# Performance work log

Hardware: AMD Instinct MI355X
Metric: run time of the kernel (lower is better)

The kernel has to match this reference:

```python
import jax, jax.numpy as jnp
import numpy as np

B, H, W, C, NB = 3, 256, 256, 16, 4
EPS = 1e-3  # keras BatchNormalization default epsilon


def _conv(x, w, b):
    y = jax.lax.conv_general_dilated(x, w, (1, 1), 'SAME',
                                     dimension_numbers=('NHWC', 'HWIO', 'NHWC'))
    return y + b


def _bn(x, g, be, mu, v):
    # inference-mode batch norm with moving statistics
    return (x - mu) * jax.lax.rsqrt(v + EPS) * g + be


def _extract_patches(x, p, s):
    # tf.image.extract_patches(..., padding='SAME') -> (b, oh, ow, p, p, c)
    b, h, w, c = x.shape
    oh, ow = -(-h // s), -(-w // s)
    pth = max((oh - 1) * s + p - h, 0)
    ptw = max((ow - 1) * s + p - w, 0)
    xp = jnp.pad(x, ((0, 0), (pth // 2, pth - pth // 2), (ptw // 2, ptw - ptw // 2), (0, 0)))
    ri = np.arange(oh)[:, None] * s + np.arange(p)[None, :]  # (oh, p)
    ci = np.arange(ow)[:, None] * s + np.arange(p)[None, :]  # (ow, p)
    return xp[:, ri[:, None, :, None], ci[None, :, None, :], :]


def setup_inputs() -> dict:
    key = jax.random.key(0)
    ks = jax.random.split(key, 4)
    mr = jax.random.normal(ks[0], (B, H, W, C), jnp.float32)
    pet = jax.random.normal(ks[1], (B, H, W, C), jnp.float32)
    W1 = jax.random.normal(ks[2], (3, 3, C, C * NB), jnp.float32) * 0.05
    W2 = jax.random.normal(ks[3], (3, 3, C * NB, C * NB), jnp.float32) * 0.05
    z = jnp.zeros((C * NB,), jnp.float32)
    o = jnp.ones((C * NB,), jnp.float32)
    return dict(mr_features=mr, pet_features=pet,
                W1=W1, b1=z, g1=o, be1=z, mu1=z, v1=o,
                W2=W2, b2=z, g2=o, be2=z, mu2=z, v2=o,
                patch=8, stride=4)


def reference(mr_features, pet_features, W1, b1, g1, be1, mu1, v1,
              W2, b2, g2, be2, mu2, v2, patch, stride):
    px = py = int(patch)
    sx = sy = int(stride)
    bsz, h, w, c = mr_features.shape

    # ---- B_Kernel_Function_Generator ----
    x = jax.nn.relu(_bn(_conv(mr_features, W1, b1), g1, be1, mu1, v1))
    x = _bn(_conv(x, W2, b2), g2, be2, mu2, v2)  # last conv_block: no activation
    nb = x.shape[-1] // c
    x = x.reshape(bsz, h, w, c, nb)
    x = jax.nn.softmax(x, axis=-1)
    b_features = jnp.where(x > 1e-5, x, 0.0)  # mask * x

    # ---- Sparse_Kernel_Matrix_Multiplication ----
    bc, bf = c, nb
    Nx, Ny = h // px, w // py
    lx, ly = px // sx, py // sy
    SNx, SNy = Nx * lx, Ny * ly

    bflat = b_features.reshape(bsz, h, w, bc * bf)
    bp = _extract_patches(bflat, px, sx).reshape(bsz, SNx, SNy, px, py, bc, bf)
    pp = _extract_patches(pet_features, px, sx).reshape(bsz, SNx, SNy, px, py, bc, 1)

    dn = jnp.sum(bp, axis=(3, 4), keepdims=True)              # diagonal norm
    kp = jnp.sum(pp * bp, axis=(3, 4), keepdims=True)         # kernel-weighted PET
    dn_safe = jnp.where(dn == 0, 1.0, dn)
    kn = jnp.where(dn == 0, 0.0, kp / dn_safe) * bp           # divide_no_nan
    kpet = jnp.sum(kn, axis=-1)                               # (b,SNx,SNy,px,py,bc)

    # deinterleave stride phases: kernel_pet[:, i::lx, j::ly] stack
    kp6 = kpet.reshape(bsz, Nx, lx, Ny, ly, px, py, c)
    st = kp6.transpose(4, 2, 0, 1, 3, 5, 6, 7).reshape(lx * ly, bsz, Nx, Ny, px, py, c)
    t = st.transpose(1, 2, 3, 4, 5, 6, 0).reshape(bsz, Nx, Ny, px, py, c, lx, ly)
    t = t.transpose(0, 1, 3, 2, 4, 5, 6, 7).reshape(bsz, Nx * px, Ny * py, c, lx, ly)
    t = t.transpose(4, 5, 0, 1, 2, 3)  # (lx, ly, b, H, W, c)

    # align_patches: roll each shifted copy back into registration, then mean
    rev = t.transpose(2, 3, 4, 5, 0, 1).reshape(bsz, h, w, c, lx * ly)
    rev = rev.transpose(4, 0, 1, 2, 3)  # (lx*ly, b, H, W, c)
    rollx = np.arange(-px // 2 + sx // 2, px // 2 + sx // 2, sx)
    rolly = np.arange(-py // 2 + sy // 2, py // 2 + sy // 2, sy)
    acc = jnp.zeros((bsz, h, w, c), rev.dtype)
    for m in range(lx * ly):  # small fixed set (lx*ly = 4)
        acc = acc + jnp.roll(rev[m], (int(rollx[m % lx]), int(rolly[m // lx])), axis=(1, 2))
    return acc / (lx * ly)
```

## Files before the change

kernel.cpp:

```cpp
#include <hip/hip_runtime.h>

#define EPSB 1e-3f

typedef _Float16 half8 __attribute__((ext_vector_type(8)));
typedef _Float16 half4 __attribute__((ext_vector_type(4)));
typedef float f32x4 __attribute__((ext_vector_type(4)));

__global__ __launch_bounds__(256, 4)
void k_prep(const float* __restrict__ W1, const float* __restrict__ W2,
            const float* __restrict__ b1, const float* __restrict__ g1,
            const float* __restrict__ be1, const float* __restrict__ mu1,
            const float* __restrict__ v1,
            const float* __restrict__ b2, const float* __restrict__ g2,
            const float* __restrict__ be2, const float* __restrict__ mu2,
            const float* __restrict__ v2,
            _Float16* __restrict__ W1F, _Float16* __restrict__ W2F,
            float* __restrict__ ST)
{
    int t = blockIdx.x * 256 + threadIdx.x;
    if (t < 5 * 4 * 64 * 8) {
        int k = t & 7, lane = (t >> 3) & 63, snt = t >> 9;
        int s = snt >> 2, ct = snt & 3;
        int quad = lane >> 4, n16 = lane & 15;
        int tap = 2 * s + (quad >> 1);
        int ci  = (quad & 1) * 8 + k;
        int co  = ct * 16 + n16;
        float v = (tap < 9) ? W1[(tap * 16 + ci) * 64 + co] : 0.f;
        W1F[t] = (_Float16)v;
        return;
    }
    t -= 5 * 4 * 64 * 8;
    if (t < 18 * 4 * 64 * 8) {
        int k = t & 7, lane = (t >> 3) & 63, snt = t >> 9;
        int s = snt >> 2, ct = snt & 3;
        int quad = lane >> 4, n16 = lane & 15;
        int tap = s >> 1;
        int ci  = (s & 1) * 32 + quad * 8 + k;
        int co  = ct * 16 + n16;
        W2F[t] = (_Float16)W2[(tap * 64 + ci) * 64 + co];
        return;
    }
    t -= 18 * 4 * 64 * 8;
    if (t < 256) {
        int c = t & 63, sel = t >> 6;
        if (sel == 0)      ST[c]       = g1[c] * rsqrtf(v1[c] + EPSB);
        else if (sel == 1) ST[64 + c]  = (b1[c] - mu1[c]) * (g1[c] * rsqrtf(v1[c] + EPSB)) + be1[c];
        else if (sel == 2) ST[128 + c] = g2[c] * rsqrtf(v2[c] + EPSB);
        else               ST[192 + c] = (b2[c] - mu2[c]) * (g2[c] * rsqrtf(v2[c] + EPSB)) + be2[c];
    }
}

#define CIP1 24
__global__ __launch_bounds__(256, 3)
void k_conv1(const float* __restrict__ mr, const _Float16* __restrict__ W1F,
             const float* __restrict__ ST, _Float16* __restrict__ A)
{
    __shared__ __align__(16) _Float16 sIn[6 * 66 * CIP1];
    const int tid = threadIdx.x;
    const int b  = blockIdx.y;
    const int r0 = (blockIdx.x >> 2) * 4;
    const int q0 = (blockIdx.x & 3) * 64;

    for (int idx = tid; idx < 6 * 66 * 2; idx += 256) {
        int c = idx & 1, pp = idx >> 1;
        int p = pp % 66, dy = pp / 66;
        int rr = r0 + dy - 1, qg = q0 + p - 1;
        half8 h = (half8)(_Float16)0.f;
        if ((unsigned)rr < 256u && (unsigned)qg < 256u) {
            const float* src = mr + ((b * 256 + rr) * 256 + qg) * 16 + c * 8;
            float4 v0 = *(const float4*)src;
            float4 v1 = *(const float4*)(src + 4);
            h = (half8){(_Float16)v0.x, (_Float16)v0.y, (_Float16)v0.z, (_Float16)v0.w,
                        (_Float16)v1.x, (_Float16)v1.y, (_Float16)v1.z, (_Float16)v1.w};
        }
        *(half8*)(&sIn[(dy * 66 + p) * CIP1 + c * 8]) = h;
    }
    __syncthreads();

    const int w = tid >> 6, lane = tid & 63;
    const int n16 = lane & 15, quad = lane >> 4;
    const int ci0 = (quad & 1) * 8;

    f32x4 acc[4][4];
    #pragma unroll
    for (int i = 0; i < 4; ++i)
        #pragma unroll
        for (int j = 0; j < 4; ++j) acc[i][j] = (f32x4){0.f, 0.f, 0.f, 0.f};

    #pragma unroll
    for (int s = 0; s < 5; ++s) {
        int tap  = 2 * s + (quad >> 1);
        int tapc = tap > 8 ? 8 : tap;
        int dy = tapc / 3, dx = tapc % 3;
        half8 wfrag[4], pfrag[4];
        #pragma unroll
        for (int ct = 0; ct < 4; ++ct)
            wfrag[ct] = *(const half8*)(W1F + ((s * 4 + ct) * 64 + lane) * 8);
        #pragma unroll
        for (int qt = 0; qt < 4; ++qt)
            pfrag[qt] = *(const half8*)&sIn[((w + dy) * 66 + qt * 16 + n16 + dx) * CIP1 + ci0];
        #pragma unroll
        for (int qt = 0; qt < 4; ++qt)
            #pragma unroll
            for (int ct = 0; ct < 4; ++ct)
                acc[qt][ct] = __builtin_amdgcn_mfma_f32_16x16x32_f16(wfrag[ct], pfrag[qt], acc[qt][ct], 0, 0, 0);
    }

    const int r = r0 + w;
    #pragma unroll
    for (int ct = 0; ct < 4; ++ct) {
        int co0 = ct * 16 + quad * 4;
        f32x4 sc = *(const f32x4*)&ST[co0];
        f32x4 sh = *(const f32x4*)&ST[64 + co0];
        #pragma unroll
        for (int qt = 0; qt < 4; ++qt) {
            int q = q0 + qt * 16 + n16;
            half4 h;
            #pragma unroll
            for (int j = 0; j < 4; ++j)
                h[j] = (_Float16)fmaxf(acc[qt][ct][j] * sc[j] + sh[j], 0.f);
            *(half4*)(A + (((b * 256 + r) * 256 + q) * 64 + co0)) = h;
        }
    }
}

#define CIP2 72
__global__ __launch_bounds__(256, 2)
void k_conv2(const _Float16* __restrict__ A, const _Float16* __restrict__ W2F,
             const float* __restrict__ ST, const float* __restrict__ pet,
             _Float16* __restrict__ BF, float* __restrict__ S2)
{
    __shared__ __align__(16) _Float16 sIn[6 * 66 * CIP2];
    const int tid = threadIdx.x;
    const int b  = blockIdx.y;
    const int r0 = (blockIdx.x >> 2) * 4;
    const int q0 = (blockIdx.x & 3) * 64;

    for (int idx = tid; idx < 6 * 66 * 8; idx += 256) {
        int c = idx & 7, pp = idx >> 3;
        int p = pp % 66, dy = pp / 66;
        int rr = r0 + dy - 1, qg = q0 + p - 1;
        int4 v = {0, 0, 0, 0};
        if ((unsigned)rr < 256u && (unsigned)qg < 256u)
            v = *(const int4*)(A + (((b * 256 + rr) * 256 + qg) * 64 + c * 8));
        *(int4*)(&sIn[(dy * 66 + p) * CIP2 + c * 8]) = v;
    }
    __syncthreads();

    const int w = tid >> 6, lane = tid & 63;
    const int n16 = lane & 15, quad = lane >> 4;

    f32x4 acc[4][4];
    #pragma unroll
    for (int i = 0; i < 4; ++i)
        #pragma unroll
        for (int j = 0; j < 4; ++j) acc[i][j] = (f32x4){0.f, 0.f, 0.f, 0.f};

    #pragma unroll
    for (int s = 0; s < 18; ++s) {
        const int tap = s >> 1;
        const int dy = tap / 3, dx = tap % 3;
        const int ci0 = (s & 1) * 32 + quad * 8;
        half8 wfrag[4], pfrag[4];
        #pragma unroll
        for (int ct = 0; ct < 4; ++ct)
            wfrag[ct] = *(const half8*)(W2F + ((s * 4 + ct) * 64 + lane) * 8);
        #pragma unroll
        for (int qt = 0; qt < 4; ++qt)
            pfrag[qt] = *(const half8*)&sIn[((w + dy) * 66 + qt * 16 + n16 + dx) * CIP2 + ci0];
        #pragma unroll
        for (int qt = 0; qt < 4; ++qt)
            #pragma unroll
            for (int ct = 0; ct < 4; ++ct)
                acc[qt][ct] = __builtin_amdgcn_mfma_f32_16x16x32_f16(wfrag[ct], pfrag[qt], acc[qt][ct], 0, 0, 0);
    }

    const int r = r0 + w;
    half4 hv[4][4];
    #pragma unroll
    for (int ct = 0; ct < 4; ++ct) {
        int co0 = ct * 16 + quad * 4;
        f32x4 sc = *(const f32x4*)&ST[128 + co0];
        f32x4 sh = *(const f32x4*)&ST[192 + co0];
        #pragma unroll
        for (int qt = 0; qt < 4; ++qt) {
            int q = q0 + qt * 16 + n16;
            float z0 = acc[qt][ct][0] * sc[0] + sh[0];
            float z1 = acc[qt][ct][1] * sc[1] + sh[1];
            float z2 = acc[qt][ct][2] * sc[2] + sh[2];
            float z3 = acc[qt][ct][3] * sc[3] + sh[3];
            float mx = fmaxf(fmaxf(z0, z1), fmaxf(z2, z3));
            float e0 = __expf(z0 - mx), e1 = __expf(z1 - mx);
            float e2 = __expf(z2 - mx), e3 = __expf(z3 - mx);
            float inv = __builtin_amdgcn_rcpf((e0 + e1) + (e2 + e3));
            float p0 = e0 * inv, p1 = e1 * inv, p2 = e2 * inv, p3 = e3 * inv;
            half4 h;
            h[0] = (_Float16)(p0 > 1e-5f ? p0 : 0.f);
            h[1] = (_Float16)(p1 > 1e-5f ? p1 : 0.f);
            h[2] = (_Float16)(p2 > 1e-5f ? p2 : 0.f);
            h[3] = (_Float16)(p3 > 1e-5f ? p3 : 0.f);
            hv[ct][qt] = h;
            *(half4*)(BF + (((b * 256 + r) * 256 + q) * 64 + co0)) = h;
        }
    }

    __syncthreads();
    #pragma unroll
    for (int ct = 0; ct < 4; ++ct) {
        int co0 = ct * 16 + quad * 4;
        #pragma unroll
        for (int qt = 0; qt < 4; ++qt) {
            int ql = qt * 16 + n16;
            *(half4*)(&sIn[(w * 64 + ql) * CIP2 + co0]) = hv[ct][qt];
        }
    }
    __syncthreads();

    const int k4 = tid & 3;
    const int cell = tid >> 2;
    const int rp = cell >> 5, qp = cell & 31;
    float dn[16], kp[16];
    #pragma unroll
    for (int j = 0; j < 16; ++j) { dn[j] = 0.f; kp[j] = 0.f; }
    #pragma unroll
    for (int u = 0; u < 2; ++u)
        #pragma unroll
        for (int v = 0; v < 2; ++v) {
            int rl = 2 * rp + u, ql = 2 * qp + v;
            half8 b0 = *(const half8*)(&sIn[(rl * 64 + ql) * CIP2 + k4 * 16]);
            half8 b1 = *(const half8*)(&sIn[(rl * 64 + ql) * CIP2 + k4 * 16 + 8]);
            float4 p4 = *(const float4*)(pet + ((b * 256 + r0 + rl) * 256 + q0 + ql) * 16 + 4 * k4);
            #pragma unroll
            for (int j = 0; j < 8; ++j) {
                float bv = (float)b0[j];
                dn[j] += bv;
                kp[j] = fmaf((j < 4) ? p4.x : p4.y, bv, kp[j]);
            }
            #pragma unroll
            for (int j = 0; j < 8; ++j) {
                float bv = (float)b1[j];
                dn[8 + j] += bv;
                kp[8 + j] = fmaf((j < 4) ? p4.z : p4.w, bv, kp[8 + j]);
            }
        }
    float* o = S2 + 2 * ((size_t)(((b * 128 + (r0 >> 1) + rp) * 128 + (q0 >> 1) + qp) * 64) + 16 * k4);
    #pragma unroll
    for (int m = 0; m < 8; ++m)
        *(float4*)(o + 4 * m) = make_float4(dn[2*m], kp[2*m], dn[2*m+1], kp[2*m+1]);
}

__global__ __launch_bounds__(256, 4)
void k_ratio(const float* __restrict__ S2, float* __restrict__ RATIO)
{
    int t = blockIdx.x * 256 + threadIdx.x;
    int cf = t & 63;
    int j  = (t >> 6) & 63;
    int i  = (t >> 12) & 63;
    int b  = t >> 18;
    float dn = 0.f, kp = 0.f;
    #pragma unroll
    for (int u = 0; u < 4; ++u) {
        int r2 = 2 * i - 1 + u;
        if ((unsigned)r2 >= 128u) continue;
        #pragma unroll
        for (int v = 0; v < 4; ++v) {
            int q2 = 2 * j - 1 + v;
            if ((unsigned)q2 >= 128u) continue;
            float2 s = *(const float2*)(S2 + 2 * (((b * 128 + r2) * 128 + q2) * 64 + cf));
            dn += s.x;
            kp += s.y;
        }
    }
    RATIO[t] = (dn == 0.f) ? 0.f : 0.25f * kp * __builtin_amdgcn_rcpf(dn);
}

__global__ __launch_bounds__(256, 4)
void k_out(const _Float16* __restrict__ BF, const float* __restrict__ RATIO,
           float* __restrict__ out)
{
    __shared__ __align__(16) float sR[2 * 64 * 68];
    const int tid = threadIdx.x;
    const int r = blockIdx.x & 255;
    const int b = blockIdx.x >> 8;

    const int i0 = (r <= 253) ? 2 * ((r + 2) >> 3)       : -1;
    const int i1 = (r >= 2)   ? 2 * ((r - 2) >> 3) + 1   : -1;

    for (int idx = tid; idx < 2048; idx += 256) {
        int ph = idx >> 10, rest = idx & 1023;
        int j = rest >> 4, c4 = rest & 15;
        int ii = ph ? i1 : i0;
        float4 v = make_float4(0.f, 0.f, 0.f, 0.f);
        if (ii >= 0)
            v = *(const float4*)&RATIO[(((b * 64 + ii) * 64 + j) << 6) + 4 * c4];
        *(float4*)&sR[(ph * 64 + j) * 68 + 4 * c4] = v;
    }
    __syncthreads();

    const int q = tid;
    const int j0 = (q <= 253) ? 2 * ((q + 2) >> 3)     : -1;
    const int j1 = (q >= 2)   ? 2 * ((q - 2) >> 3) + 1 : -1;

    const half8* bfp = (const half8*)(BF + ((size_t)(b * 256 + r) * 256 + q) * 64);
    float o[16];
    #pragma unroll
    for (int c = 0; c < 16; ++c) o[c] = 0.f;

    #pragma unroll
    for (int c2 = 0; c2 < 8; ++c2) {
        half8 bf8 = bfp[c2];
        float s0 = 0.f, s1 = 0.f;
        #pragma unroll
        for (int pi = 0; pi < 2; ++pi) {
            #pragma unroll
            for (int pj = 0; pj < 2; ++pj) {
                int jj = pj ? j1 : j0;
                if (jj < 0) continue;
                const float* rp_ = &sR[(pi * 64 + jj) * 68 + 8 * c2];
                s0 += (float)bf8[0] * rp_[0] + (float)bf8[1] * rp_[1]
                    + (float)bf8[2] * rp_[2] + (float)bf8[3] * rp_[3];
                s1 += (float)bf8[4] * rp_[4] + (float)bf8[5] * rp_[5]
                    + (float)bf8[6] * rp_[6] + (float)bf8[7] * rp_[7];
            }
        }
        o[2 * c2]     = s0;
        o[2 * c2 + 1] = s1;
    }
    float* op = out + ((size_t)(b * 256 + r) * 256 + q) * 16;
    #pragma unroll
    for (int m = 0; m < 4; ++m)
        *(float4*)(op + 4 * m) = make_float4(o[4*m], o[4*m+1], o[4*m+2], o[4*m+3]);
}

extern "C" void kernel_launch(void* const* d_in, const int* in_sizes, int n_in,
                              void* d_out, int out_size, void* d_ws, size_t ws_size,
                              hipStream_t stream) {
    const float* mr  = (const float*)d_in[0];
    const float* pet = (const float*)d_in[1];
    const float* W1  = (const float*)d_in[2];
    const float* b1  = (const float*)d_in[3];
    const float* g1  = (const float*)d_in[4];
    const float* be1 = (const float*)d_in[5];
    const float* mu1 = (const float*)d_in[6];
    const float* v1  = (const float*)d_in[7];
    const float* W2  = (const float*)d_in[8];
    const float* b2  = (const float*)d_in[9];
    const float* g2  = (const float*)d_in[10];
    const float* be2 = (const float*)d_in[11];
    const float* mu2 = (const float*)d_in[12];
    const float* v2  = (const float*)d_in[13];

    char* ws = (char*)d_ws;
    _Float16* A     = (_Float16*)(ws);
    _Float16* BF    = (_Float16*)(ws + 25165824);
    float*    S2    = (float*)(ws + 50331648);
    float*    RATIO = (float*)(ws + 75497472);
    _Float16* W1F   = (_Float16*)(ws + 78643200);
    _Float16* W2F   = (_Float16*)(ws + 78663680);
    float*    ST    = (float*)(ws + 78737408);
    float*    out   = (float*)d_out;

    dim3 blk(256);
    k_prep<<<185, blk, 0, stream>>>(W1, W2, b1, g1, be1, mu1, v1,
                                    b2, g2, be2, mu2, v2, W1F, W2F, ST);
    k_conv1<<<dim3(256, 3), blk, 0, stream>>>(mr, W1F, ST, A);
    k_conv2<<<dim3(256, 3), blk, 0, stream>>>(A, W2F, ST, pet, BF, S2);
    k_ratio<<<3072, blk, 0, stream>>>(S2, RATIO);
    k_out<<<768, blk, 0, stream>>>(BF, RATIO, out);
}
```

Baseline: 177.1 us.

## Halve conv row tiles, split warps across columns, stage outputs through LDS

```diff
diff --git a/kernel.cpp b/kernel.cpp
--- a/kernel.cpp
+++ b/kernel.cpp
@@ -51,17 +51,17 @@
 }
 
 #define CIP1 24
-__global__ __launch_bounds__(256, 3)
+__global__ __launch_bounds__(256, 4)
 void k_conv1(const float* __restrict__ mr, const _Float16* __restrict__ W1F,
              const float* __restrict__ ST, _Float16* __restrict__ A)
 {
-    __shared__ __align__(16) _Float16 sIn[6 * 66 * CIP1];
+    __shared__ __align__(16) _Float16 sM[2 * 64 * 72];
     const int tid = threadIdx.x;
     const int b  = blockIdx.y;
-    const int r0 = (blockIdx.x >> 2) * 4;
+    const int r0 = (blockIdx.x >> 2) * 2;
     const int q0 = (blockIdx.x & 3) * 64;
 
-    for (int idx = tid; idx < 6 * 66 * 2; idx += 256) {
+    for (int idx = tid; idx < 4 * 66 * 2; idx += 256) {
         int c = idx & 1, pp = idx >> 1;
         int p = pp % 66, dy = pp / 66;
         int rr = r0 + dy - 1, qg = q0 + p - 1;
@@ -73,17 +73,18 @@
             h = (half8){(_Float16)v0.x, (_Float16)v0.y, (_Float16)v0.z, (_Float16)v0.w,
                         (_Float16)v1.x, (_Float16)v1.y, (_Float16)v1.z, (_Float16)v1.w};
         }
-        *(half8*)(&sIn[(dy * 66 + p) * CIP1 + c * 8]) = h;
+        *(half8*)(&sM[(dy * 66 + p) * CIP1 + c * 8]) = h;
     }
     __syncthreads();
 
     const int w = tid >> 6, lane = tid & 63;
     const int n16 = lane & 15, quad = lane >> 4;
+    const int rl = w >> 1, qh = (w & 1) * 32;
     const int ci0 = (quad & 1) * 8;
 
-    f32x4 acc[4][4];
-    #pragma unroll
-    for (int i = 0; i < 4; ++i)
+    f32x4 acc[2][4];
+    #pragma unroll
+    for (int i = 0; i < 2; ++i)
         #pragma unroll
         for (int j = 0; j < 4; ++j) acc[i][j] = (f32x4){0.f, 0.f, 0.f, 0.f};
 
@@ -92,67 +93,85 @@
         int tap  = 2 * s + (quad >> 1);
         int tapc = tap > 8 ? 8 : tap;
         int dy = tapc / 3, dx = tapc % 3;
-        half8 wfrag[4], pfrag[4];
+        half8 wfrag[4], pfrag[2];
         #pragma unroll
         for (int ct = 0; ct < 4; ++ct)
             wfrag[ct] = *(const half8*)(W1F + ((s * 4 + ct) * 64 + lane) * 8);
         #pragma unroll
-        for (int qt = 0; qt < 4; ++qt)
-            pfrag[qt] = *(const half8*)&sIn[((w + dy) * 66 + qt * 16 + n16 + dx) * CIP1 + ci0];
-        #pragma unroll
-        for (int qt = 0; qt < 4; ++qt)
+        for (int qt = 0; qt < 2; ++qt)
+            pfrag[qt] = *(const half8*)&sM[((rl + dy) * 66 + qh + qt * 16 + n16 + dx) * CIP1 + ci0];
+        #pragma unroll
+        for (int qt = 0; qt < 2; ++qt)
             #pragma unroll
             for (int ct = 0; ct < 4; ++ct)
                 acc[qt][ct] = __builtin_amdgcn_mfma_f32_16x16x32_f16(wfrag[ct], pfrag[qt], acc[qt][ct], 0, 0, 0);
     }
 
-    const int r = r0 + w;
+    half4 hv[4][2];
     #pragma unroll
     for (int ct = 0; ct < 4; ++ct) {
         int co0 = ct * 16 + quad * 4;
         f32x4 sc = *(const f32x4*)&ST[co0];
         f32x4 sh = *(const f32x4*)&ST[64 + co0];
         #pragma unroll
-        for (int qt = 0; qt < 4; ++qt) {
-            int q = q0 + qt * 16 + n16;
+        for (int qt = 0; qt < 2; ++qt) {
             half4 h;
             #pragma unroll
             for (int j = 0; j < 4; ++j)
                 h[j] = (_Float16)fmaxf(acc[qt][ct][j] * sc[j] + sh[j], 0.f);
-            *(half4*)(A + (((b * 256 + r) * 256 + q) * 64 + co0)) = h;
-        }
+            hv[ct][qt] = h;
+        }
+    }
+    __syncthreads();
+    #pragma unroll
+    for (int ct = 0; ct < 4; ++ct) {
+        int co0 = ct * 16 + quad * 4;
+        #pragma unroll
+        for (int qt = 0; qt < 2; ++qt) {
+            int ql = qh + qt * 16 + n16;
+            *(half4*)(&sM[(rl * 64 + ql) * 72 + co0]) = hv[ct][qt];
+        }
+    }
+    __syncthreads();
+
+    for (int idx = tid; idx < 1024; idx += 256) {
+        int rl2 = idx >> 9, rest = idx & 511;
+        int ql = rest >> 3, seg = rest & 7;
+        int4 v = *(const int4*)&sM[(rl2 * 64 + ql) * 72 + seg * 8];
+        *(int4*)(A + (((b * 256 + r0 + rl2) * 256 + q0 + ql) * 64 + seg * 8)) = v;
     }
 }
 
 #define CIP2 72
-__global__ __launch_bounds__(256, 2)
+__global__ __launch_bounds__(256, 4)
 void k_conv2(const _Float16* __restrict__ A, const _Float16* __restrict__ W2F,
              const float* __restrict__ ST, const float* __restrict__ pet,
              _Float16* __restrict__ BF, float* __restrict__ S2)
 {
-    __shared__ __align__(16) _Float16 sIn[6 * 66 * CIP2];
+    __shared__ __align__(16) _Float16 sM[4 * 66 * CIP2];
     const int tid = threadIdx.x;
     const int b  = blockIdx.y;
-    const int r0 = (blockIdx.x >> 2) * 4;
+    const int r0 = (blockIdx.x >> 2) * 2;
     const int q0 = (blockIdx.x & 3) * 64;
 
-    for (int idx = tid; idx < 6 * 66 * 8; idx += 256) {
+    for (int idx = tid; idx < 4 * 66 * 8; idx += 256) {
         int c = idx & 7, pp = idx >> 3;
         int p = pp % 66, dy = pp / 66;
         int rr = r0 + dy - 1, qg = q0 + p - 1;
         int4 v = {0, 0, 0, 0};
         if ((unsigned)rr < 256u && (unsigned)qg < 256u)
             v = *(const int4*)(A + (((b * 256 + rr) * 256 + qg) * 64 + c * 8));
-        *(int4*)(&sIn[(dy * 66 + p) * CIP2 + c * 8]) = v;
+        *(int4*)(&sM[(dy * 66 + p) * CIP2 + c * 8]) = v;
     }
     __syncthreads();
 
     const int w = tid >> 6, lane = tid & 63;
     const int n16 = lane & 15, quad = lane >> 4;
-
-    f32x4 acc[4][4];
-    #pragma unroll
-    for (int i = 0; i < 4; ++i)
+    const int rl = w >> 1, qh = (w & 1) * 32;
+
+    f32x4 acc[2][4];
+    #pragma unroll
+    for (int i = 0; i < 2; ++i)
         #pragma unroll
         for (int j = 0; j < 4; ++j) acc[i][j] = (f32x4){0.f, 0.f, 0.f, 0.f};
 
@@ -161,30 +180,28 @@
         const int tap = s >> 1;
         const int dy = tap / 3, dx = tap % 3;
         const int ci0 = (s & 1) * 32 + quad * 8;
-        half8 wfrag[4], pfrag[4];
+        half8 wfrag[4], pfrag[2];
         #pragma unroll
         for (int ct = 0; ct < 4; ++ct)
             wfrag[ct] = *(const half8*)(W2F + ((s * 4 + ct) * 64 + lane) * 8);
         #pragma unroll
-        for (int qt = 0; qt < 4; ++qt)
-            pfrag[qt] = *(const half8*)&sIn[((w + dy) * 66 + qt * 16 + n16 + dx) * CIP2 + ci0];
-        #pragma unroll
-        for (int qt = 0; qt < 4; ++qt)
+        for (int qt = 0; qt < 2; ++qt)
+            pfrag[qt] = *(const half8*)&sM[((rl + dy) * 66 + qh + qt * 16 + n16 + dx) * CIP2 + ci0];
+        #pragma unroll
+        for (int qt = 0; qt < 2; ++qt)
             #pragma unroll
             for (int ct = 0; ct < 4; ++ct)
                 acc[qt][ct] = __builtin_amdgcn_mfma_f32_16x16x32_f16(wfrag[ct], pfrag[qt], acc[qt][ct], 0, 0, 0);
     }
 
-    const int r = r0 + w;
-    half4 hv[4][4];
+    half4 hv[4][2];
     #pragma unroll
     for (int ct = 0; ct < 4; ++ct) {
         int co0 = ct * 16 + quad * 4;
         f32x4 sc = *(const f32x4*)&ST[128 + co0];
         f32x4 sh = *(const f32x4*)&ST[192 + co0];
         #pragma unroll
-        for (int qt = 0; qt < 4; ++qt) {
-            int q = q0 + qt * 16 + n16;
+        for (int qt = 0; qt < 2; ++qt) {
             float z0 = acc[qt][ct][0] * sc[0] + sh[0];
             float z1 = acc[qt][ct][1] * sc[1] + sh[1];
             float z2 = acc[qt][ct][2] * sc[2] + sh[2];
@@ -200,52 +217,48 @@
             h[2] = (_Float16)(p2 > 1e-5f ? p2 : 0.f);
             h[3] = (_Float16)(p3 > 1e-5f ? p3 : 0.f);
             hv[ct][qt] = h;
-            *(half4*)(BF + (((b * 256 + r) * 256 + q) * 64 + co0)) = h;
-        }
-    }
-
+        }
+    }
     __syncthreads();
     #pragma unroll
     for (int ct = 0; ct < 4; ++ct) {
         int co0 = ct * 16 + quad * 4;
         #pragma unroll
-        for (int qt = 0; qt < 4; ++qt) {
-            int ql = qt * 16 + n16;
-            *(half4*)(&sIn[(w * 64 + ql) * CIP2 + co0]) = hv[ct][qt];
-        }
-    }
-    __syncthreads();
-
-    const int k4 = tid & 3;
-    const int cell = tid >> 2;
-    const int rp = cell >> 5, qp = cell & 31;
-    float dn[16], kp[16];
-    #pragma unroll
-    for (int j = 0; j < 16; ++j) { dn[j] = 0.f; kp[j] = 0.f; }
+        for (int qt = 0; qt < 2; ++qt) {
+            int ql = qh + qt * 16 + n16;
+            *(half4*)(&sM[(rl * 64 + ql) * CIP2 + co0]) = hv[ct][qt];
+        }
+    }
+    __syncthreads();
+
+    for (int idx = tid; idx < 1024; idx += 256) {
+        int rl2 = idx >> 9, rest = idx & 511;
+        int ql = rest >> 3, seg = rest & 7;
+        int4 v = *(const int4*)&sM[(rl2 * 64 + ql) * CIP2 + seg * 8];
+        *(int4*)(BF + (((b * 256 + r0 + rl2) * 256 + q0 + ql) * 64 + seg * 8)) = v;
+    }
+
+    const int qp = tid >> 3, chg = tid & 7;
+    float dn[8], kp[8];
+    #pragma unroll
+    for (int j = 0; j < 8; ++j) { dn[j] = 0.f; kp[j] = 0.f; }
     #pragma unroll
     for (int u = 0; u < 2; ++u)
         #pragma unroll
         for (int v = 0; v < 2; ++v) {
-            int rl = 2 * rp + u, ql = 2 * qp + v;
-            half8 b0 = *(const half8*)(&sIn[(rl * 64 + ql) * CIP2 + k4 * 16]);
-            half8 b1 = *(const half8*)(&sIn[(rl * 64 + ql) * CIP2 + k4 * 16 + 8]);
-            float4 p4 = *(const float4*)(pet + ((b * 256 + r0 + rl) * 256 + q0 + ql) * 16 + 4 * k4);
+            int ql = 2 * qp + v;
+            half8 bf = *(const half8*)(&sM[(u * 64 + ql) * CIP2 + chg * 8]);
+            float2 p2 = *(const float2*)(pet + ((b * 256 + r0 + u) * 256 + q0 + ql) * 16 + chg * 2);
             #pragma unroll
             for (int j = 0; j < 8; ++j) {
-                float bv = (float)b0[j];
+                float bv = (float)bf[j];
                 dn[j] += bv;
-                kp[j] = fmaf((j < 4) ? p4.x : p4.y, bv, kp[j]);
+                kp[j] = fmaf((j < 4) ? p2.x : p2.y, bv, kp[j]);
             }
-            #pragma unroll
-            for (int j = 0; j < 8; ++j) {
-                float bv = (float)b1[j];
-                dn[8 + j] += bv;
-                kp[8 + j] = fmaf((j < 4) ? p4.z : p4.w, bv, kp[8 + j]);
-            }
-        }
-    float* o = S2 + 2 * ((size_t)(((b * 128 + (r0 >> 1) + rp) * 128 + (q0 >> 1) + qp) * 64) + 16 * k4);
-    #pragma unroll
-    for (int m = 0; m < 8; ++m)
+        }
+    float* o = S2 + 2 * ((size_t)(((b * 128 + (r0 >> 1)) * 128 + (q0 >> 1) + qp) * 64) + chg * 8);
+    #pragma unroll
+    for (int m = 0; m < 4; ++m)
         *(float4*)(o + 4 * m) = make_float4(dn[2*m], kp[2*m], dn[2*m+1], kp[2*m+1]);
 }
 
@@ -363,8 +376,8 @@
     dim3 blk(256);
     k_prep<<<185, blk, 0, stream>>>(W1, W2, b1, g1, be1, mu1, v1,
                                     b2, g2, be2, mu2, v2, W1F, W2F, ST);
-    k_conv1<<<dim3(256, 3), blk, 0, stream>>>(mr, W1F, ST, A);
-    k_conv2<<<dim3(256, 3), blk, 0, stream>>>(A, W2F, ST, pet, BF, S2);
+    k_conv1<<<dim3(512, 3), blk, 0, stream>>>(mr, W1F, ST, A);
+    k_conv2<<<dim3(512, 3), blk, 0, stream>>>(A, W2F, ST, pet, BF, S2);
     k_ratio<<<3072, blk, 0, stream>>>(S2, RATIO);
     k_out<<<768, blk, 0, stream>>>(BF, RATIO, out);
 }
```

After: 171.7 us. 1.03x faster.

## Stage conv outputs through LDS for coalesced stores, pre-sum ratio phases

Applied to the files above, without the earlier changes.

```diff
diff --git a/kernel.cpp b/kernel.cpp
--- a/kernel.cpp
+++ b/kernel.cpp
@@ -55,7 +55,7 @@
 void k_conv1(const float* __restrict__ mr, const _Float16* __restrict__ W1F,
              const float* __restrict__ ST, _Float16* __restrict__ A)
 {
-    __shared__ __align__(16) _Float16 sIn[6 * 66 * CIP1];
+    __shared__ __align__(16) _Float16 sM[4 * 64 * 72];
     const int tid = threadIdx.x;
     const int b  = blockIdx.y;
     const int r0 = (blockIdx.x >> 2) * 4;
@@ -73,7 +73,7 @@
             h = (half8){(_Float16)v0.x, (_Float16)v0.y, (_Float16)v0.z, (_Float16)v0.w,
                         (_Float16)v1.x, (_Float16)v1.y, (_Float16)v1.z, (_Float16)v1.w};
         }
-        *(half8*)(&sIn[(dy * 66 + p) * CIP1 + c * 8]) = h;
+        *(half8*)(&sM[(dy * 66 + p) * CIP1 + c * 8]) = h;
     }
     __syncthreads();
 
@@ -98,7 +98,7 @@
             wfrag[ct] = *(const half8*)(W1F + ((s * 4 + ct) * 64 + lane) * 8);
         #pragma unroll
         for (int qt = 0; qt < 4; ++qt)
-            pfrag[qt] = *(const half8*)&sIn[((w + dy) * 66 + qt * 16 + n16 + dx) * CIP1 + ci0];
+            pfrag[qt] = *(const half8*)&sM[((w + dy) * 66 + qt * 16 + n16 + dx) * CIP1 + ci0];
         #pragma unroll
         for (int qt = 0; qt < 4; ++qt)
             #pragma unroll
@@ -106,7 +106,7 @@
                 acc[qt][ct] = __builtin_amdgcn_mfma_f32_16x16x32_f16(wfrag[ct], pfrag[qt], acc[qt][ct], 0, 0, 0);
     }
 
-    const int r = r0 + w;
+    half4 hv[4][4];
     #pragma unroll
     for (int ct = 0; ct < 4; ++ct) {
         int co0 = ct * 16 + quad * 4;
@@ -114,13 +114,30 @@
         f32x4 sh = *(const f32x4*)&ST[64 + co0];
         #pragma unroll
         for (int qt = 0; qt < 4; ++qt) {
-            int q = q0 + qt * 16 + n16;
             half4 h;
             #pragma unroll
             for (int j = 0; j < 4; ++j)
                 h[j] = (_Float16)fmaxf(acc[qt][ct][j] * sc[j] + sh[j], 0.f);
-            *(half4*)(A + (((b * 256 + r) * 256 + q) * 64 + co0)) = h;
-        }
+            hv[ct][qt] = h;
+        }
+    }
+    __syncthreads();
+    #pragma unroll
+    for (int ct = 0; ct < 4; ++ct) {
+        int co0 = ct * 16 + quad * 4;
+        #pragma unroll
+        for (int qt = 0; qt < 4; ++qt) {
+            int ql = qt * 16 + n16;
+            *(half4*)(&sM[(w * 64 + ql) * 72 + co0]) = hv[ct][qt];
+        }
+    }
+    __syncthreads();
+
+    for (int idx = tid; idx < 2048; idx += 256) {
+        int rl2 = idx >> 9, rest = idx & 511;
+        int ql = rest >> 3, seg = rest & 7;
+        int4 v = *(const int4*)&sM[(rl2 * 64 + ql) * 72 + seg * 8];
+        *(int4*)(A + (((b * 256 + r0 + rl2) * 256 + q0 + ql) * 64 + seg * 8)) = v;
     }
 }
 
@@ -130,7 +147,7 @@
              const float* __restrict__ ST, const float* __restrict__ pet,
              _Float16* __restrict__ BF, float* __restrict__ S2)
 {
-    __shared__ __align__(16) _Float16 sIn[6 * 66 * CIP2];
+    __shared__ __align__(16) _Float16 sM[6 * 66 * CIP2];
     const int tid = threadIdx.x;
     const int b  = blockIdx.y;
     const int r0 = (blockIdx.x >> 2) * 4;
@@ -143,7 +160,7 @@
         int4 v = {0, 0, 0, 0};
         if ((unsigned)rr < 256u && (unsigned)qg < 256u)
             v = *(const int4*)(A + (((b * 256 + rr) * 256 + qg) * 64 + c * 8));
-        *(int4*)(&sIn[(dy * 66 + p) * CIP2 + c * 8]) = v;
+        *(int4*)(&sM[(dy * 66 + p) * CIP2 + c * 8]) = v;
     }
     __syncthreads();
 
@@ -167,7 +184,7 @@
             wfrag[ct] = *(const half8*)(W2F + ((s * 4 + ct) * 64 + lane) * 8);
         #pragma unroll
         for (int qt = 0; qt < 4; ++qt)
-            pfrag[qt] = *(const half8*)&sIn[((w + dy) * 66 + qt * 16 + n16 + dx) * CIP2 + ci0];
+            pfrag[qt] = *(const half8*)&sM[((w + dy) * 66 + qt * 16 + n16 + dx) * CIP2 + ci0];
         #pragma unroll
         for (int qt = 0; qt < 4; ++qt)
             #pragma unroll
@@ -175,7 +192,6 @@
                 acc[qt][ct] = __builtin_amdgcn_mfma_f32_16x16x32_f16(wfrag[ct], pfrag[qt], acc[qt][ct], 0, 0, 0);
     }
 
-    const int r = r0 + w;
     half4 hv[4][4];
     #pragma unroll
     for (int ct = 0; ct < 4; ++ct) {
@@ -184,7 +200,6 @@
         f32x4 sh = *(const f32x4*)&ST[192 + co0];
         #pragma unroll
         for (int qt = 0; qt < 4; ++qt) {
-            int q = q0 + qt * 16 + n16;
             float z0 = acc[qt][ct][0] * sc[0] + sh[0];
             float z1 = acc[qt][ct][1] * sc[1] + sh[1];
             float z2 = acc[qt][ct][2] * sc[2] + sh[2];
@@ -200,10 +215,8 @@
             h[2] = (_Float16)(p2 > 1e-5f ? p2 : 0.f);
             h[3] = (_Float16)(p3 > 1e-5f ? p3 : 0.f);
             hv[ct][qt] = h;
-            *(half4*)(BF + (((b * 256 + r) * 256 + q) * 64 + co0)) = h;
-        }
-    }
-
+        }
+    }
     __syncthreads();
     #pragma unroll
     for (int ct = 0; ct < 4; ++ct) {
@@ -211,42 +224,43 @@
         #pragma unroll
         for (int qt = 0; qt < 4; ++qt) {
             int ql = qt * 16 + n16;
-            *(half4*)(&sIn[(w * 64 + ql) * CIP2 + co0]) = hv[ct][qt];
-        }
-    }
-    __syncthreads();
-
-    const int k4 = tid & 3;
-    const int cell = tid >> 2;
-    const int rp = cell >> 5, qp = cell & 31;
-    float dn[16], kp[16];
-    #pragma unroll
-    for (int j = 0; j < 16; ++j) { dn[j] = 0.f; kp[j] = 0.f; }
-    #pragma unroll
-    for (int u = 0; u < 2; ++u)
-        #pragma unroll
-        for (int v = 0; v < 2; ++v) {
-            int rl = 2 * rp + u, ql = 2 * qp + v;
-            half8 b0 = *(const half8*)(&sIn[(rl * 64 + ql) * CIP2 + k4 * 16]);
-            half8 b1 = *(const half8*)(&sIn[(rl * 64 + ql) * CIP2 + k4 * 16 + 8]);
-            float4 p4 = *(const float4*)(pet + ((b * 256 + r0 + rl) * 256 + q0 + ql) * 16 + 4 * k4);
+            *(half4*)(&sM[(w * 64 + ql) * CIP2 + co0]) = hv[ct][qt];
+        }
+    }
+    __syncthreads();
+
+    for (int idx = tid; idx < 2048; idx += 256) {
+        int rl2 = idx >> 9, rest = idx & 511;
+        int ql = rest >> 3, seg = rest & 7;
+        int4 v = *(const int4*)&sM[(rl2 * 64 + ql) * CIP2 + seg * 8];
+        *(int4*)(BF + (((b * 256 + r0 + rl2) * 256 + q0 + ql) * 64 + seg * 8)) = v;
+    }
+
+    const int qp = tid >> 3, chg = tid & 7;
+    #pragma unroll
+    for (int cr = 0; cr < 2; ++cr) {
+        float dn[8], kp[8];
+        #pragma unroll
+        for (int j = 0; j < 8; ++j) { dn[j] = 0.f; kp[j] = 0.f; }
+        #pragma unroll
+        for (int u = 0; u < 2; ++u)
             #pragma unroll
-            for (int j = 0; j < 8; ++j) {
-                float bv = (float)b0[j];
-                dn[j] += bv;
-                kp[j] = fmaf((j < 4) ? p4.x : p4.y, bv, kp[j]);
+            for (int v = 0; v < 2; ++v) {
+                int rl = 2 * cr + u, ql = 2 * qp + v;
+                half8 bf = *(const half8*)(&sM[(rl * 64 + ql) * CIP2 + chg * 8]);
+                float2 p2 = *(const float2*)(pet + ((b * 256 + r0 + rl) * 256 + q0 + ql) * 16 + chg * 2);
+                #pragma unroll
+                for (int j = 0; j < 8; ++j) {
+                    float bv = (float)bf[j];
+                    dn[j] += bv;
+                    kp[j] = fmaf((j < 4) ? p2.x : p2.y, bv, kp[j]);
+                }
             }
-            #pragma unroll
-            for (int j = 0; j < 8; ++j) {
-                float bv = (float)b1[j];
-                dn[8 + j] += bv;
-                kp[8 + j] = fmaf((j < 4) ? p4.z : p4.w, bv, kp[8 + j]);
-            }
-        }
-    float* o = S2 + 2 * ((size_t)(((b * 128 + (r0 >> 1) + rp) * 128 + (q0 >> 1) + qp) * 64) + 16 * k4);
-    #pragma unroll
-    for (int m = 0; m < 8; ++m)
-        *(float4*)(o + 4 * m) = make_float4(dn[2*m], kp[2*m], dn[2*m+1], kp[2*m+1]);
+        float* o = S2 + 2 * ((size_t)(((b * 128 + (r0 >> 1) + cr) * 128 + (q0 >> 1) + qp) * 64) + chg * 8);
+        #pragma unroll
+        for (int m = 0; m < 4; ++m)
+            *(float4*)(o + 4 * m) = make_float4(dn[2*m], kp[2*m], dn[2*m+1], kp[2*m+1]);
+    }
 }
 
 __global__ __launch_bounds__(256, 4)
@@ -278,7 +292,7 @@
 void k_out(const _Float16* __restrict__ BF, const float* __restrict__ RATIO,
            float* __restrict__ out)
 {
-    __shared__ __align__(16) float sR[2 * 64 * 68];
+    __shared__ __align__(16) float sU[64 * 68];
     const int tid = threadIdx.x;
     const int r = blockIdx.x & 255;
     const int b = blockIdx.x >> 8;
@@ -286,14 +300,13 @@
     const int i0 = (r <= 253) ? 2 * ((r + 2) >> 3)       : -1;
     const int i1 = (r >= 2)   ? 2 * ((r - 2) >> 3) + 1   : -1;
 
-    for (int idx = tid; idx < 2048; idx += 256) {
-        int ph = idx >> 10, rest = idx & 1023;
-        int j = rest >> 4, c4 = rest & 15;
-        int ii = ph ? i1 : i0;
-        float4 v = make_float4(0.f, 0.f, 0.f, 0.f);
-        if (ii >= 0)
-            v = *(const float4*)&RATIO[(((b * 64 + ii) * 64 + j) << 6) + 4 * c4];
-        *(float4*)&sR[(ph * 64 + j) * 68 + 4 * c4] = v;
+    for (int idx = tid; idx < 1024; idx += 256) {
+        int j = idx >> 4, c4 = idx & 15;
+        float4 a = make_float4(0.f, 0.f, 0.f, 0.f);
+        if (i0 >= 0) a = *(const float4*)&RATIO[(((b * 64 + i0) * 64 + j) << 6) + 4 * c4];
+        float4 bb = make_float4(0.f, 0.f, 0.f, 0.f);
+        if (i1 >= 0) bb = *(const float4*)&RATIO[(((b * 64 + i1) * 64 + j) << 6) + 4 * c4];
+        *(float4*)&sU[j * 68 + 4 * c4] = make_float4(a.x + bb.x, a.y + bb.y, a.z + bb.z, a.w + bb.w);
     }
     __syncthreads();
 
@@ -311,17 +324,14 @@
         half8 bf8 = bfp[c2];
         float s0 = 0.f, s1 = 0.f;
         #pragma unroll
-        for (int pi = 0; pi < 2; ++pi) {
-            #pragma unroll
-            for (int pj = 0; pj < 2; ++pj) {
-                int jj = pj ? j1 : j0;
-                if (jj < 0) continue;
-                const float* rp_ = &sR[(pi * 64 + jj) * 68 + 8 * c2];
-                s0 += (float)bf8[0] * rp_[0] + (float)bf8[1] * rp_[1]
-                    + (float)bf8[2] * rp_[2] + (float)bf8[3] * rp_[3];
-                s1 += (float)bf8[4] * rp_[4] + (float)bf8[5] * rp_[5]
-                    + (float)bf8[6] * rp_[6] + (float)bf8[7] * rp_[7];
-            }
+        for (int pj = 0; pj < 2; ++pj) {
+            int jj = pj ? j1 : j0;
+            if (jj < 0) continue;
+            const float* up = &sU[jj * 68 + 8 * c2];
+            s0 += (float)bf8[0] * up[0] + (float)bf8[1] * up[1]
+                + (float)bf8[2] * up[2] + (float)bf8[3] * up[3];
+            s1 += (float)bf8[4] * up[4] + (float)bf8[5] * up[5]
+                + (float)bf8[6] * up[6] + (float)bf8[7] * up[7];
         }
         o[2 * c2]     = s0;
         o[2 * c2 + 1] = s1;
```

Result: faster. 173.2 us (-2.2%).
